# Optimization experiments

Hardware: AMD Instinct MI355X
Metric: run time of the kernel (lower is better)

The kernel has to match this reference:

```python
import jax, jax.numpy as jnp
import numpy as np

N, E = 20000, 320000
CS, CV = 64, 32            # 64x0e + 32x1o node irreps
CM = CS + CV               # mid scalar channels == mid vector channels == 96
WN = 2 * CS + 2 * CV       # tp weight numel per edge (4 uvu instructions) = 192
FCH = 64                   # fc hidden width
SQRT3 = 1.7320508075688772


def _fctp(s, v, attr, Ws, Wv):
    # FullyConnectedTensorProduct(x, attr='1x0e', out): per-l linear scaled by the scalar attr
    out_s = (s @ Ws) * attr / (s.shape[1] ** 0.5)
    out_v = jnp.einsum('nuc,uw->nwc', v, Wv) * attr[:, :, None] / (v.shape[1] ** 0.5)
    return out_s, out_v


def _fcnet(x, Wa, Wb):
    # FullyConnectedNet([64, 64, WN], silu)
    h = jax.nn.silu(x @ Wa / (x.shape[1] ** 0.5))
    return h @ Wb / (h.shape[1] ** 0.5)


def _conv(s, v, attr, edge_src, edge_dst, ea_s, ea_v, edge_scalars, inv_sqrt_deg, params):
    Wsc_s, Wsc_v, Wl1_s, Wl1_v, Wfa, Wfb, W2s, W2v, W3 = params
    n = s.shape[0]
    w = _fcnet(edge_scalars, Wfa, Wfb)                      # [E, 192] per-edge tp weights
    w00, w01, w10, w11 = w[:, :CS], w[:, CS:2 * CS], w[:, 2 * CS:2 * CS + CV], w[:, 2 * CS + CV:]
    sc_s, sc_v = _fctp(s, v, attr, Wsc_s, Wsc_v)            # self connection
    f_s, f_v = _fctp(s, v, attr, Wl1_s, Wl1_v)              # lin1
    gs, gv = f_s[edge_src], f_v[edge_src]                   # gather by edge source
    # weighted CG tensor product (uvu), sorted irreps_mid = 96x0e + 96x1o
    mid_s = jnp.concatenate([
        w00 * gs * ea_s,                                    # 0e x 0e -> 0e
        w11 * jnp.einsum('euc,ec->eu', gv, ea_v) / SQRT3,   # 1o x 1o -> 0e
    ], axis=-1)                                             # [E, 96]
    mid_v = jnp.concatenate([
        (w01 * gs)[:, :, None] * ea_v[:, None, :],          # 0e x 1o -> 1o
        w10[:, :, None] * gv * ea_s[:, :, None],            # 1o x 0e -> 1o
    ], axis=1)                                              # [E, 96, 3]
    agg_s = jax.ops.segment_sum(mid_s, edge_dst, num_segments=n) * inv_sqrt_deg
    agg_v = jax.ops.segment_sum(mid_v, edge_dst, num_segments=n) * inv_sqrt_deg[:, :, None]
    fan = CM ** 0.5
    out_s = (agg_s @ W2s) * attr / fan                      # lin2
    out_v = jnp.einsum('nuc,uw->nwc', agg_v, W2v) * attr[:, :, None] / fan
    angle = 0.1 * (agg_s @ W3) * attr / fan                 # lin3 -> '0e'
    c, si = jnp.cos(angle), jnp.sin(angle)                  # sc output_mask is all-ones here
    return c * sc_s + si * out_s, c[:, :, None] * sc_v + si[:, :, None] * out_v


def _forward(node_features, node_attr, edge_attr, edge_scalars, edge_src, edge_dst, params1, params2):
    n = node_features.shape[0]
    s = node_features[:, :CS]
    v = node_features[:, CS:].reshape(n, CV, 3)
    ea_s, ea_v = edge_attr[:, :1], edge_attr[:, 1:4]
    deg = jax.ops.segment_sum(jnp.ones((edge_dst.shape[0],), node_features.dtype), edge_dst, num_segments=n)
    inv_sqrt_deg = (1.0 / jnp.sqrt(deg))[:, None]           # every node has >= 1 in-edge by construction
    h_s, h_v = _conv(s, v, node_attr, edge_src, edge_dst, ea_s, ea_v, edge_scalars, inv_sqrt_deg, params1)
    # Gate: 64x0e scalars (silu) + 32x0e gates (sigmoid) gating 32x1o
    g_s = jax.nn.silu(h_s[:, :CS])
    g_v = jax.nn.sigmoid(h_s[:, CS:CS + CV])[:, :, None] * h_v
    o_s, o_v = _conv(g_s, g_v, node_attr, edge_src, edge_dst, ea_s, ea_v, edge_scalars, inv_sqrt_deg, params2)
    return jnp.concatenate([o_s, o_v.reshape(n, CV * 3)], axis=-1)


def setup_inputs():
    key = jax.random.key(0)
    ks = jax.random.split(key, 24)
    inp = {
        'node_features': jax.random.normal(ks[0], (N, CS + 3 * CV), jnp.float32),
        'node_attr': jnp.ones((N, 1), jnp.float32),
        'edge_src': jax.random.randint(ks[1], (E,), 0, N, dtype=jnp.int32),
        'edge_dst': jnp.concatenate([jnp.arange(N, dtype=jnp.int32),
                                     jax.random.randint(ks[2], (E - N,), 0, N, dtype=jnp.int32)]),
        'edge_attr': jax.random.normal(ks[3], (E, 4), jnp.float32),
        'edge_scalars': jax.random.normal(ks[4], (E, CS), jnp.float32),
    }
    shapes = {
        'p1_sc_s': (CS, CS + CV), 'p1_sc_v': (CV, CV),
        'p1_l1_s': (CS, CS), 'p1_l1_v': (CV, CV),
        'p1_fa': (CS, FCH), 'p1_fb': (FCH, WN),
        'p1_l2_s': (CM, CS + CV), 'p1_l2_v': (CM, CV), 'p1_l3': (CM, 1),
        'p2_sc_s': (CS, CS), 'p2_sc_v': (CV, CV),
        'p2_l1_s': (CS, CS), 'p2_l1_v': (CV, CV),
        'p2_fa': (CS, FCH), 'p2_fb': (FCH, WN),
        'p2_l2_s': (CM, CS), 'p2_l2_v': (CM, CV), 'p2_l3': (CM, 1),
    }
    for i, (name, shp) in enumerate(shapes.items()):
        inp[name] = jax.random.normal(ks[5 + i], shp, jnp.float32)
    return inp


def reference(node_features, node_attr, edge_attr, edge_scalars, edge_src, edge_dst,
              p1_sc_s, p1_sc_v, p1_l1_s, p1_l1_v, p1_fa, p1_fb, p1_l2_s, p1_l2_v, p1_l3,
              p2_sc_s, p2_sc_v, p2_l1_s, p2_l1_v, p2_fa, p2_fb, p2_l2_s, p2_l2_v, p2_l3):
    params1 = (p1_sc_s, p1_sc_v, p1_l1_s, p1_l1_v, p1_fa, p1_fb, p1_l2_s, p1_l2_v, p1_l3)
    params2 = (p2_sc_s, p2_sc_v, p2_l1_s, p2_l1_v, p2_fa, p2_fb, p2_l2_s, p2_l2_v, p2_l3)
    return _forward(node_features, node_attr, edge_attr, edge_scalars, edge_src, edge_dst, params1, params2)
```

## Files before the change

### kernel.cpp

```cpp
#include <hip/hip_runtime.h>
#include <hip/hip_fp16.h>
#include <cstdint>


#define CS 64
#define CV 32
#define CM 96
#define WN 192
#define FCH 64
#define WPAD 72
#define CHUNK 64
#define NSLABS 2

using f16x8 = __attribute__((ext_vector_type(8))) _Float16;
using f32x4 = __attribute__((ext_vector_type(4))) float;

__device__ __forceinline__ float siluf(float x){ return x / (1.f + __expf(-x)); }

constexpr float INV8       = 0.125f;
constexpr float INV_SQRT32 = 0.17677669529663687f;
constexpr float INV_SQRT96 = 0.10206207261596575f;
constexpr float INV_SQRT3  = 0.5773502691896258f;

__global__ void hist_kernel(const int* __restrict__ edst, int* __restrict__ cnt, int E){
    int e = blockIdx.x*blockDim.x + threadIdx.x;
    if (e < E) atomicAdd(&cnt[edst[e]], 1);
}

__global__ void scan_kernel(const int* __restrict__ cnt, int* __restrict__ row_start,
                            int* __restrict__ cursor, int n, int E){
    __shared__ int part[1024];
    const int t = threadIdx.x;
    const int C = (n + 1023) / 1024;
    int local[32];
    int base = t*C;
    int s = 0;
    for (int j = 0; j < C && j < 32; ++j){
        int idx = base + j;
        int v = (idx < n) ? cnt[idx] : 0;
        local[j] = s; s += v;
    }
    part[t] = s;
    __syncthreads();
    for (int off = 1; off < 1024; off <<= 1){
        int v = (t >= off) ? part[t-off] : 0;
        __syncthreads();
        part[t] += v;
        __syncthreads();
    }
    int pre = (t == 0) ? 0 : part[t-1];
    for (int j = 0; j < C && j < 32; ++j){
        int idx = base + j;
        if (idx < n){ int rs = pre + local[j]; row_start[idx] = rs; cursor[idx] = rs; }
    }
    if (t == 0) row_start[n] = E;
}

__global__ void scatter_kernel(const int* __restrict__ edst, const int* __restrict__ esrc,
                               const float4* __restrict__ eattr,
                               int* __restrict__ cursor, int* __restrict__ perm,
                               float4* __restrict__ eattr_s, int* __restrict__ esrc_s, int E){
    int e = blockIdx.x*blockDim.x + threadIdx.x;
    if (e < E){
        int p = atomicAdd(&cursor[edst[e]], 1);
        perm[p] = e; eattr_s[p] = eattr[e]; esrc_s[p] = esrc[e];
    }
}

__global__ void isd_kernel(const int* __restrict__ cnt, float* __restrict__ isd, int n){
    int i = blockIdx.x*blockDim.x + threadIdx.x;
    if (i < n) isd[i] = rsqrtf((float)cnt[i]);
}

__global__ void wprep(const float* __restrict__ Wfa1, const float* __restrict__ Wfb1,
                      const float* __restrict__ Wfa2, const float* __restrict__ Wfb2,
                      __half* __restrict__ Wc1, __half* __restrict__ Wc2){
    int t = blockIdx.x*blockDim.x + threadIdx.x;
    if (t < 64*WPAD){
        int c = t / WPAD, k = t - c*WPAD;
        float v1 = (k < 64) ? Wfa1[k*64 + c]*INV8 : 0.f;
        float v2 = (k < 64) ? Wfa2[k*64 + c]*INV8 : 0.f;
        Wc1[t] = __float2half(v1); Wc2[t] = __float2half(v2);
    } else if (t < 64*WPAD + 192*WPAD){
        int q = t - 64*WPAD; int o = q / WPAD, k = q - o*WPAD;
        float v1 = (k < 64) ? Wfb1[k*192 + o]*INV8 : 0.f;
        float v2 = (k < 64) ? Wfb2[k*192 + o]*INV8 : 0.f;
        Wc1[t] = __float2half(v1); Wc2[t] = __float2half(v2);
    }
}

__global__ void wprep_pre(
    const float* __restrict__ l1s1, const float* __restrict__ scs1,
    const float* __restrict__ l1v1, const float* __restrict__ scv1,
    const float* __restrict__ l1s2, const float* __restrict__ scs2,
    const float* __restrict__ l1v2, const float* __restrict__ scv2,
    __half* __restrict__ Bs1, __half* __restrict__ Bs2,
    __half* __restrict__ Bv1, __half* __restrict__ Bv2)
{
    int t = blockIdx.x*blockDim.x + threadIdx.x;
    if (t < 160*72){
        int col = t/72, k = t - col*72;
        float v = 0.f;
        if (k < 64) v = (col < 64 ? l1s1[k*64 + col] : scs1[k*96 + (col-64)]) * INV8;
        Bs1[t] = __float2half(v);
    } else if (t < 160*72 + 128*72){
        int q = t - 160*72; int col = q/72, k = q - col*72;
        float v = 0.f;
        if (k < 64) v = (col < 64 ? l1s2[k*64 + col] : scs2[k*64 + (col-64)]) * INV8;
        Bs2[q] = __float2half(v);
    } else if (t < 160*72 + 128*72 + 64*40){
        int q = t - (160*72 + 128*72); int col = q/40, k = q - col*40;
        float v = 0.f;
        if (k < 32) v = (col < 32 ? l1v1[k*32 + col] : scv1[k*32 + (col-32)]) * INV_SQRT32;
        Bv1[q] = __float2half(v);
    } else if (t < 160*72 + 128*72 + 2*64*40){
        int q = t - (160*72 + 128*72 + 64*40); int col = q/40, k = q - col*40;
        float v = 0.f;
        if (k < 32) v = (col < 32 ? l1v2[k*32 + col] : scv2[k*32 + (col-32)]) * INV_SQRT32;
        Bv2[q] = __float2half(v);
    }
}

template<int OS>
__global__ __launch_bounds__(256) void node_pre_mfma(
    const float* __restrict__ s, int ss,
    const float* __restrict__ v, int vs,
    const float* __restrict__ attr,
    const __half* __restrict__ Bs, const __half* __restrict__ Bv,
    __half* __restrict__ f_s, float* __restrict__ sc_s,
    __half* __restrict__ f_v, float* __restrict__ sc_v, int N)
{
    constexpr int SC = 64 + OS;
    __shared__ __align__(16) __half sAh[64*168];
    __shared__ __align__(16) __half lBs[SC*72];
    __shared__ __align__(16) __half lBv[64*40];
    __shared__ float s_at[64];

    const int tid = threadIdx.x;
    const int n0 = blockIdx.x*64;
    const int nmax = min(64, N - n0);

    for (int i = tid; i < (SC*72)/8; i += 256)
        reinterpret_cast<uint4*>(lBs)[i] = reinterpret_cast<const uint4*>(Bs)[i];
    for (int i = tid; i < (64*40)/8; i += 256)
        reinterpret_cast<uint4*>(lBv)[i] = reinterpret_cast<const uint4*>(Bv)[i];
    for (int i = tid; i < 64*64; i += 256){
        int n = i >> 6, k = i & 63;
        float x = (n < nmax) ? s[(size_t)(n0+n)*ss + k] : 0.f;
        sAh[n*168 + k] = __float2half(x);
    }
    for (int i = tid; i < 64*96; i += 256){
        int n = i/96, k = i - n*96;
        float x = (n < nmax) ? v[(size_t)(n0+n)*vs + k] : 0.f;
        sAh[n*168 + 64 + k] = __float2half(x);
    }
    if (tid < 64) s_at[tid] = (tid < nmax) ? attr[n0 + tid] : 0.f;
    __syncthreads();

    const int wv = tid >> 6, l = tid & 63;
    const int lm = l & 15, kg = l >> 4;
    const int rbase = wv*16;
    const int orow = rbase + kg*4;

    f16x8 xf0 = *reinterpret_cast<const f16x8*>(&sAh[(rbase+lm)*168 + kg*8]);
    f16x8 xf1 = *reinterpret_cast<const f16x8*>(&sAh[(rbase+lm)*168 + 32 + kg*8]);
    #pragma unroll
    for (int nt = 0; nt < SC/16; ++nt){
        f16x8 wb0 = *reinterpret_cast<const f16x8*>(&lBs[(nt*16+lm)*72 + kg*8]);
        f16x8 wb1 = *reinterpret_cast<const f16x8*>(&lBs[(nt*16+lm)*72 + 32 + kg*8]);
        f32x4 acc = {0.f,0.f,0.f,0.f};
        acc = __builtin_amdgcn_mfma_f32_16x16x32_f16(xf0, wb0, acc, 0, 0, 0);
        acc = __builtin_amdgcn_mfma_f32_16x16x32_f16(xf1, wb1, acc, 0, 0, 0);
        const int col = nt*16 + lm;
        #pragma unroll
        for (int r = 0; r < 4; ++r){
            int nl = orow + r;
            if (nl < nmax){
                float val = acc[r]*s_at[nl];
                if (col < 64) f_s[(size_t)(n0+nl)*64 + col] = __float2half(val);
                else          sc_s[(size_t)(n0+nl)*OS + (col-64)] = val;
            }
        }
    }

    #pragma unroll
    for (int c = 0; c < 3; ++c){
        f16x8 xa;
        #pragma unroll
        for (int j = 0; j < 8; ++j)
            xa[j] = (_Float16)sAh[(rbase+lm)*168 + 64 + (kg*8+j)*3 + c];
        #pragma unroll
        for (int nt = 0; nt < 4; ++nt){
            f16x8 wb = *reinterpret_cast<const f16x8*>(&lBv[(nt*16+lm)*40 + kg*8]);
            f32x4 acc = {0.f,0.f,0.f,0.f};
            acc = __builtin_amdgcn_mfma_f32_16x16x32_f16(xa, wb, acc, 0, 0, 0);
            const int col = nt*16 + lm;
            #pragma unroll
            for (int r = 0; r < 4; ++r){
                int nl = orow + r;
                if (nl < nmax){
                    float val = acc[r]*s_at[nl];
                    if (col < 32) f_v[(size_t)(n0+nl)*96 + col*3 + c] = __float2half(val);
                    else          sc_v[(size_t)(n0+nl)*96 + (col-32)*3 + c] = val;
                }
            }
        }
    }
}

__global__ __launch_bounds__(256) void mlp_gemm_slab(
    const int* __restrict__ row_start, int n0, int n1,
    const int* __restrict__ perm, const float* __restrict__ escal,
    const __half* __restrict__ Wc, __half* __restrict__ w_slab, int E)
{
    __shared__ __half lWa[64*WPAD];
    __shared__ __half lWb[192*WPAD];
    __shared__ __half hsm[4][16*WPAD];

    const int rs_slab = row_start[n0];
    const int re_slab = row_start[n1];
    if (rs_slab + (int)blockIdx.x*64 >= re_slab) return;

    const int tid = threadIdx.x;
    {
        const uint4* src4 = reinterpret_cast<const uint4*>(Wc);
        uint4* dA = reinterpret_cast<uint4*>(lWa);
        uint4* dB = reinterpret_cast<uint4*>(lWb);
        for (int i = tid; i < (64*WPAD)/8; i += 256) dA[i] = src4[i];
        for (int i = tid; i < (192*WPAD)/8; i += 256) dB[i] = src4[(64*WPAD)/8 + i];
    }
    __syncthreads();

    const int wv = tid >> 6, l = tid & 63;
    const int lm = l & 15, kg = l >> 4;

    for (int tile = rs_slab + blockIdx.x*64; tile < re_slab; tile += gridDim.x*64){
        const int base = tile + wv*16;
        int slot = base + lm; if (slot >= re_slab) slot = re_slab - 1;
        const int e = perm[slot];
        const float* xp = escal + (size_t)e*64 + kg*8;
        f16x8 xf0, xf1;
        {
            float4 a0 = *reinterpret_cast<const float4*>(xp);
            float4 a1 = *reinterpret_cast<const float4*>(xp + 4);
            float4 b0 = *reinterpret_cast<const float4*>(xp + 32);
            float4 b1 = *reinterpret_cast<const float4*>(xp + 36);
            xf0[0]=(_Float16)a0.x; xf0[1]=(_Float16)a0.y; xf0[2]=(_Float16)a0.z; xf0[3]=(_Float16)a0.w;
            xf0[4]=(_Float16)a1.x; xf0[5]=(_Float16)a1.y; xf0[6]=(_Float16)a1.z; xf0[7]=(_Float16)a1.w;
            xf1[0]=(_Float16)b0.x; xf1[1]=(_Float16)b0.y; xf1[2]=(_Float16)b0.z; xf1[3]=(_Float16)b0.w;
            xf1[4]=(_Float16)b1.x; xf1[5]=(_Float16)b1.y; xf1[6]=(_Float16)b1.z; xf1[7]=(_Float16)b1.w;
        }

        #pragma unroll
        for (int nt = 0; nt < 4; ++nt){
            f16x8 wa0 = *reinterpret_cast<const f16x8*>(&lWa[(nt*16 + lm)*WPAD + kg*8]);
            f16x8 wa1 = *reinterpret_cast<const f16x8*>(&lWa[(nt*16 + lm)*WPAD + 32 + kg*8]);
            f32x4 acc = {0.f,0.f,0.f,0.f};
            acc = __builtin_amdgcn_mfma_f32_16x16x32_f16(xf0, wa0, acc, 0, 0, 0);
            acc = __builtin_amdgcn_mfma_f32_16x16x32_f16(xf1, wa1, acc, 0, 0, 0);
            #pragma unroll
            for (int r = 0; r < 4; ++r)
                hsm[wv][(kg*4 + r)*WPAD + nt*16 + lm] = __float2half(siluf(acc[r]));
        }
        f16x8 ha0 = *reinterpret_cast<const f16x8*>(&hsm[wv][lm*WPAD + kg*8]);
        f16x8 ha1 = *reinterpret_cast<const f16x8*>(&hsm[wv][lm*WPAD + 32 + kg*8]);
        const int orow = base + kg*4;
        #pragma unroll 4
        for (int nt = 0; nt < 12; ++nt){
            f16x8 wb0 = *reinterpret_cast<const f16x8*>(&lWb[(nt*16 + lm)*WPAD + kg*8]);
            f16x8 wb1 = *reinterpret_cast<const f16x8*>(&lWb[(nt*16 + lm)*WPAD + 32 + kg*8]);
            f32x4 acc = {0.f,0.f,0.f,0.f};
            acc = __builtin_amdgcn_mfma_f32_16x16x32_f16(ha0, wb0, acc, 0, 0, 0);
            acc = __builtin_amdgcn_mfma_f32_16x16x32_f16(ha1, wb1, acc, 0, 0, 0);
            #pragma unroll
            for (int r = 0; r < 4; ++r){
                int row = orow + r;
                if (row < re_slab)
                    w_slab[(size_t)(row - rs_slab)*WN + nt*16 + lm] = __float2half(acc[r]);
            }
        }
    }
}

__global__ __launch_bounds__(384) void agg_slab(
    const int* __restrict__ row_start, int n0, const __half* __restrict__ w_slab,
    const int* __restrict__ esrc_s, const float4* __restrict__ eattr_s,
    const __half* __restrict__ f_s, const __half* __restrict__ f_v,
    float* __restrict__ aggs, float* __restrict__ aggv, int N)
{
    const int n = n0 + blockIdx.x;
    if (n >= N) return;
    const int t = threadIdx.x;
    const int rs_slab = row_start[n0];
    const int rs = row_start[n], re = row_start[n+1];
    const size_t N96 = (size_t)N*96;

    int widx, fidx, mode, eac = 0;
    float* outp;
    if (t < 64){ widx = t; fidx = t; mode = 0; eac = 0; outp = aggs + (size_t)n*96 + t; }
    else if (t < 256){ int j = t-64; int c = j>>6; int u = j&63;
        widx = 64+u; fidx = u; mode = 0; eac = 1+c; outp = aggv + (size_t)c*N96 + (size_t)n*96 + u; }
    else if (t < 352){ int j = t-256; int c = j>>5; int u = j&31;
        widx = 128+u; fidx = 3*u+c; mode = 2; outp = aggv + (size_t)c*N96 + (size_t)n*96 + 64+u; }
    else { int u = t-352; widx = 160+u; fidx = 3*u; mode = 1; outp = aggs + (size_t)n*96 + 64+u; }

    __shared__ int   s_src[CHUNK];
    __shared__ float s_ea[4][CHUNK];

    float acc = 0.f;
    for (int c0 = rs; c0 < re; c0 += CHUNK){
        const int m = min(CHUNK, re - c0);
        __syncthreads();
        if (t < m){
            s_src[t] = esrc_s[c0 + t];
            float4 ea = eattr_s[c0 + t];
            s_ea[0][t] = ea.x; s_ea[1][t] = ea.y;
            s_ea[2][t] = ea.z; s_ea[3][t] = ea.w;
        }
        __syncthreads();

        const __half* wp = w_slab + (size_t)(c0 - rs_slab)*WN + widx;
        if (mode == 0){
            int i = 0;
            for (; i + 8 <= m; i += 8){
                float w8[8], g8[8], e8[8];
                #pragma unroll
                for (int k = 0; k < 8; ++k) w8[k] = __half2float(wp[(i+k)*WN]);
                #pragma unroll
                for (int k = 0; k < 8; ++k) g8[k] = __half2float(f_s[(size_t)s_src[i+k]*64 + fidx]);
                #pragma unroll
                for (int k = 0; k < 8; ++k) e8[k] = s_ea[eac][i+k];
                #pragma unroll
                for (int k = 0; k < 8; ++k) acc += w8[k]*g8[k]*e8[k];
            }
            for (; i < m; ++i)
                acc += __half2float(wp[i*WN]) * __half2float(f_s[(size_t)s_src[i]*64 + fidx]) * s_ea[eac][i];
        } else if (mode == 2){
            int i = 0;
            for (; i + 8 <= m; i += 8){
                float w8[8], g8[8], e8[8];
                #pragma unroll
                for (int k = 0; k < 8; ++k) w8[k] = __half2float(wp[(i+k)*WN]);
                #pragma unroll
                for (int k = 0; k < 8; ++k) g8[k] = __half2float(f_v[(size_t)s_src[i+k]*96 + fidx]);
                #pragma unroll
                for (int k = 0; k < 8; ++k) e8[k] = s_ea[0][i+k];
                #pragma unroll
                for (int k = 0; k < 8; ++k) acc += w8[k]*g8[k]*e8[k];
            }
            for (; i < m; ++i)
                acc += __half2float(wp[i*WN]) * __half2float(f_v[(size_t)s_src[i]*96 + fidx]) * s_ea[0][i];
        } else {
            int i = 0;
            for (; i + 4 <= m; i += 4){
                float w4[4], d4[4];
                #pragma unroll
                for (int k = 0; k < 4; ++k) w4[k] = __half2float(wp[(i+k)*WN]);
                #pragma unroll
                for (int k = 0; k < 4; ++k){
                    const __half* p = f_v + (size_t)s_src[i+k]*96 + fidx;
                    d4[k] = __half2float(p[0])*s_ea[1][i+k] + __half2float(p[1])*s_ea[2][i+k]
                          + __half2float(p[2])*s_ea[3][i+k];
                }
                #pragma unroll
                for (int k = 0; k < 4; ++k) acc += w4[k]*d4[k];
            }
            for (; i < m; ++i){
                const __half* p = f_v + (size_t)s_src[i]*96 + fidx;
                float d = __half2float(p[0])*s_ea[1][i] + __half2float(p[1])*s_ea[2][i]
                        + __half2float(p[2])*s_ea[3][i];
                acc += __half2float(wp[i*WN]) * d;
            }
            acc *= INV_SQRT3;
        }
    }
    *outp = acc;
}

template<int OS, bool FINAL>
__global__ __launch_bounds__(256) void post_fused(
    const float* __restrict__ aggs, const float* __restrict__ aggv,
    const float* __restrict__ W2s, const float* __restrict__ W2v,
    const float* __restrict__ W3,
    const float* __restrict__ isd, const float* __restrict__ attr,
    const float* __restrict__ sc_s, const float* __restrict__ sc_v,
    float* __restrict__ out_s, float* __restrict__ out_v, int N)
{
    constexpr int TOTC = OS + 1 + 96;
    constexpr int PSTR = 96*8 + 8;
    __shared__ __align__(16) float s_a[4*PSTR];
    __shared__ float s_pre[8][TOTC];

    const int t = threadIdx.x;
    const int n0 = blockIdx.x*8;
    const int nmax = min(8, N - n0);
    const size_t N96 = (size_t)N*96;

    for (int idx = t; idx < 8*96; idx += 256){
        int n = idx/96, k = idx - n*96;
        if (n < nmax) s_a[k*8 + n] = aggs[(size_t)(n0+n)*96 + k];
    }
    for (int idx = t; idx < 3*8*96; idx += 256){
        int p = idx/768, rem = idx - p*768;
        int n = rem/96, k = rem - n*96;
        if (n < nmax) s_a[(1+p)*PSTR + k*8 + n] = aggv[(size_t)p*N96 + (size_t)(n0+n)*96 + k];
    }
    __syncthreads();

    if (t < TOTC){
        const float* bp; int bstr; int plane;
        if (t < OS){ bp = W2s + t; bstr = OS; plane = 0; }
        else if (t == OS){ bp = W3; bstr = 1; plane = 0; }
        else { int q = t - OS - 1; int cv = q>>5, ww = q&31; bp = W2v + ww; bstr = 32; plane = 1+cv; }
        const float* ap = &s_a[plane*PSTR];

        float acc0=0,acc1=0,acc2=0,acc3=0,acc4=0,acc5=0,acc6=0,acc7=0;
        #pragma unroll 4
        for (int k = 0; k < 96; ++k){
            float b = bp[(size_t)k*bstr];
            float4 q0 = *reinterpret_cast<const float4*>(ap + k*8);
            float4 q1 = *reinterpret_cast<const float4*>(ap + k*8 + 4);
            acc0 += q0.x*b; acc1 += q0.y*b; acc2 += q0.z*b; acc3 += q0.w*b;
            acc4 += q1.x*b; acc5 += q1.y*b; acc6 += q1.z*b; acc7 += q1.w*b;
        }
        s_pre[0][t]=acc0; s_pre[1][t]=acc1; s_pre[2][t]=acc2; s_pre[3][t]=acc3;
        s_pre[4][t]=acc4; s_pre[5][t]=acc5; s_pre[6][t]=acc6; s_pre[7][t]=acc7;
    }
    __syncthreads();

    for (int idx = t; idx < nmax*192; idx += 256){
        int n = idx/192, r = idx - n*192;
        int gn = n0 + n;
        float sca = isd[gn]*attr[gn]*INV_SQRT96;
        float ang = 0.1f * s_pre[n][OS] * sca;
        float c_ = cosf(ang), s_ = sinf(ang);
        if (r < OS){
            float hs = c_*sc_s[(size_t)gn*OS + r] + s_*s_pre[n][r]*sca;
            if (FINAL) out_s[(size_t)gn*160 + r] = hs;
            else if (r < 64) out_s[(size_t)gn*64 + r] = siluf(hs);
        } else if (r >= 96){
            int q2 = r - 96;
            int ww = q2/3, c2 = q2 - 3*ww;
            float hv = c_*sc_v[(size_t)gn*96 + q2] + s_*s_pre[n][OS+1 + c2*32 + ww]*sca;
            if (FINAL){
                out_s[(size_t)gn*160 + 64 + q2] = hv;
            } else {
                float hs64 = c_*sc_s[(size_t)gn*OS + 64 + ww] + s_*s_pre[n][64 + ww]*sca;
                float sg = 1.f/(1.f + __expf(-hs64));
                out_v[(size_t)gn*96 + q2] = sg*hv;
            }
        }
    }
}

extern "C" void kernel_launch(void* const* d_in, const int* in_sizes, int n_in,
                              void* d_out, int out_size, void* d_ws, size_t ws_size,
                              hipStream_t stream)
{
    const float* nf    = (const float*)d_in[0];
    const float* nattr = (const float*)d_in[1];
    const int*   esrc  = (const int*)  d_in[2];
    const int*   edst  = (const int*)  d_in[3];
    const float* eattr = (const float*)d_in[4];
    const float* escal = (const float*)d_in[5];
    const float* p1_sc_s = (const float*)d_in[6];
    const float* p1_sc_v = (const float*)d_in[7];
    const float* p1_l1_s = (const float*)d_in[8];
    const float* p1_l1_v = (const float*)d_in[9];
    const float* p1_fa   = (const float*)d_in[10];
    const float* p1_fb   = (const float*)d_in[11];
    const float* p1_l2_s = (const float*)d_in[12];
    const float* p1_l2_v = (const float*)d_in[13];
    const float* p1_l3   = (const float*)d_in[14];
    const float* p2_sc_s = (const float*)d_in[15];
    const float* p2_sc_v = (const float*)d_in[16];
    const float* p2_l1_s = (const float*)d_in[17];
    const float* p2_l1_v = (const float*)d_in[18];
    const float* p2_fa   = (const float*)d_in[19];
    const float* p2_fb   = (const float*)d_in[20];
    const float* p2_l2_s = (const float*)d_in[21];
    const float* p2_l2_v = (const float*)d_in[22];
    const float* p2_l3   = (const float*)d_in[23];

    const int N = in_sizes[1];
    const int E = in_sizes[2];

    char* wsb = (char*)d_ws;
    __half* w_s     = (__half*)wsb;   wsb += (size_t)E*WN*2;
    float4* eattr_s = (float4*)wsb;   wsb += (size_t)E*16;
    __half* Wc1 = (__half*)wsb;       wsb += (size_t)(256*WPAD)*2;
    __half* Wc2 = (__half*)wsb;       wsb += (size_t)(256*WPAD)*2;
    __half* Bs1 = (__half*)wsb;       wsb += (size_t)(160*72)*2;
    __half* Bs2 = (__half*)wsb;       wsb += (size_t)(128*72)*2;
    __half* Bv1 = (__half*)wsb;       wsb += (size_t)(64*40)*2;
    __half* Bv2 = (__half*)wsb;       wsb += (size_t)(64*40)*2;
    __half* fs  = (__half*)wsb;       wsb += (size_t)N*64*2;
    __half* fv  = (__half*)wsb;       wsb += (size_t)N*96*2;
    float* scs  = (float*)wsb;        wsb += (size_t)N*96*4;
    float* scv  = (float*)wsb;        wsb += (size_t)N*96*4;
    float* gs   = (float*)wsb;        wsb += (size_t)N*64*4;
    float* gv   = (float*)wsb;        wsb += (size_t)N*96*4;
    float* aggs = (float*)wsb;        wsb += (size_t)N*96*4;
    float* aggv = (float*)wsb;        wsb += (size_t)N*96*3*4;
    float* isd  = (float*)wsb;        wsb += (size_t)N*4;
    int* cnt       = (int*)wsb;       wsb += (size_t)N*4;
    int* row_start = (int*)wsb;       wsb += (size_t)(N+1)*4;
    int* cursor    = (int*)wsb;       wsb += (size_t)N*4;
    int* perm      = (int*)wsb;       wsb += (size_t)E*4;
    int* esrc_s    = (int*)wsb;       wsb += (size_t)E*4;

    hipMemsetAsync(cnt, 0, (size_t)N*4, stream);
    hist_kernel<<<(E+255)/256, 256, 0, stream>>>(edst, cnt, E);
    scan_kernel<<<1, 1024, 0, stream>>>(cnt, row_start, cursor, N, E);
    scatter_kernel<<<(E+255)/256, 256, 0, stream>>>(edst, esrc, (const float4*)eattr,
                                                    cursor, perm, eattr_s, esrc_s, E);
    isd_kernel<<<(N+255)/256, 256, 0, stream>>>(cnt, isd, N);
    wprep<<<(256*WPAD+255)/256, 256, 0, stream>>>(p1_fa, p1_fb, p2_fa, p2_fb, Wc1, Wc2);
    wprep_pre<<<(160*72+128*72+2*64*40+255)/256, 256, 0, stream>>>(
        p1_l1_s, p1_sc_s, p1_l1_v, p1_sc_v,
        p2_l1_s, p2_sc_s, p2_l1_v, p2_sc_v, Bs1, Bs2, Bv1, Bv2);

    const int pre_grid  = (N + 63)/64;
    const int post_grid = (N + 7)/8;
    const int slabN = (N + NSLABS - 1)/NSLABS;
    const int mlp_grid = 768;

    node_pre_mfma<96><<<pre_grid, 256, 0, stream>>>(nf, 160, nf+64, 160, nattr,
        Bs1, Bv1, fs, scs, fv, scv, N);
    for (int s = 0; s < NSLABS; ++s){
        int n0 = s*slabN; if (n0 >= N) break;
        int n1 = (n0 + slabN < N) ? n0 + slabN : N;
        mlp_gemm_slab<<<mlp_grid, 256, 0, stream>>>(row_start, n0, n1, perm, escal,
                                                    Wc1, w_s, E);
        agg_slab<<<n1 - n0, 384, 0, stream>>>(row_start, n0, w_s,
                                              esrc_s, eattr_s, fs, fv, aggs, aggv, N);
    }
    post_fused<96, false><<<post_grid, 256, 0, stream>>>(aggs, aggv,
        p1_l2_s, p1_l2_v, p1_l3, isd, nattr, scs, scv, gs, gv, N);

    node_pre_mfma<64><<<pre_grid, 256, 0, stream>>>(gs, 64, gv, 96, nattr,
        Bs2, Bv2, fs, scs, fv, scv, N);
    for (int s = 0; s < NSLABS; ++s){
        int n0 = s*slabN; if (n0 >= N) break;
        int n1 = (n0 + slabN < N) ? n0 + slabN : N;
        mlp_gemm_slab<<<mlp_grid, 256, 0, stream>>>(row_start, n0, n1, perm, escal,
                                                    Wc2, w_s, E);
        agg_slab<<<n1 - n0, 384, 0, stream>>>(row_start, n0, w_s,
                                              esrc_s, eattr_s, fs, fv, aggs, aggv, N);
    }
    post_fused<64, true><<<post_grid, 256, 0, stream>>>(aggs, aggv,
        p2_l2_s, p2_l2_v, p2_l3, isd, nattr, scs, scv, (float*)d_out, nullptr, N);
}
```

Baseline: 475.9 us.

## Compute four outputs per thread in agg_slab to reuse gathered features

The aggregation kernel now runs 128 threads per node instead of 384. Each thread keeps four accumulators: scalar threads handle one channel for the 0e×0e output and all three 1o components from the same gathered f_s value, and vector threads handle the three 0e×1o components plus the dot-product scalar from one gathered 3-vector. This removes repeated gathers of the same source features and repeated shared-memory reads across threads. In exchange there are fewer threads per block, a third of them sit idle (threads 96–127), and each thread has more serial work, so latency hiding may drop.

New measurement: 385.8 us (median of 2 runs). -18.9%, faster.

```diff
diff --git a/kernel.cpp b/kernel.cpp
--- a/kernel.cpp
+++ b/kernel.cpp
@@ -282,7 +282,7 @@
     }
 }
 
-__global__ __launch_bounds__(384) void agg_slab(
+__global__ __launch_bounds__(128) void agg_slab(
     const int* __restrict__ row_start, int n0, const __half* __restrict__ w_slab,
     const int* __restrict__ esrc_s, const float4* __restrict__ eattr_s,
     const __half* __restrict__ f_s, const __half* __restrict__ f_v,
@@ -295,19 +295,14 @@
     const int rs = row_start[n], re = row_start[n+1];
     const size_t N96 = (size_t)N*96;
 
-    int widx, fidx, mode, eac = 0;
-    float* outp;
-    if (t < 64){ widx = t; fidx = t; mode = 0; eac = 0; outp = aggs + (size_t)n*96 + t; }
-    else if (t < 256){ int j = t-64; int c = j>>6; int u = j&63;
-        widx = 64+u; fidx = u; mode = 0; eac = 1+c; outp = aggv + (size_t)c*N96 + (size_t)n*96 + u; }
-    else if (t < 352){ int j = t-256; int c = j>>5; int u = j&31;
-        widx = 128+u; fidx = 3*u+c; mode = 2; outp = aggv + (size_t)c*N96 + (size_t)n*96 + 64+u; }
-    else { int u = t-352; widx = 160+u; fidx = 3*u; mode = 1; outp = aggs + (size_t)n*96 + 64+u; }
-
     __shared__ int   s_src[CHUNK];
     __shared__ float s_ea[4][CHUNK];
 
-    float acc = 0.f;
+    const bool isScalar = (t < 64);
+    const int u = t - 64;
+
+    float a0 = 0.f, a1 = 0.f, a2 = 0.f, a3 = 0.f;
+
     for (int c0 = rs; c0 < re; c0 += CHUNK){
         const int m = min(CHUNK, re - c0);
         __syncthreads();
@@ -319,62 +314,91 @@
         }
         __syncthreads();
 
-        const __half* wp = w_slab + (size_t)(c0 - rs_slab)*WN + widx;
-        if (mode == 0){
-            int i = 0;
-            for (; i + 8 <= m; i += 8){
-                float w8[8], g8[8], e8[8];
-                #pragma unroll
-                for (int k = 0; k < 8; ++k) w8[k] = __half2float(wp[(i+k)*WN]);
-                #pragma unroll
-                for (int k = 0; k < 8; ++k) g8[k] = __half2float(f_s[(size_t)s_src[i+k]*64 + fidx]);
-                #pragma unroll
-                for (int k = 0; k < 8; ++k) e8[k] = s_ea[eac][i+k];
-                #pragma unroll
-                for (int k = 0; k < 8; ++k) acc += w8[k]*g8[k]*e8[k];
-            }
-            for (; i < m; ++i)
-                acc += __half2float(wp[i*WN]) * __half2float(f_s[(size_t)s_src[i]*64 + fidx]) * s_ea[eac][i];
-        } else if (mode == 2){
-            int i = 0;
-            for (; i + 8 <= m; i += 8){
-                float w8[8], g8[8], e8[8];
-                #pragma unroll
-                for (int k = 0; k < 8; ++k) w8[k] = __half2float(wp[(i+k)*WN]);
-                #pragma unroll
-                for (int k = 0; k < 8; ++k) g8[k] = __half2float(f_v[(size_t)s_src[i+k]*96 + fidx]);
-                #pragma unroll
-                for (int k = 0; k < 8; ++k) e8[k] = s_ea[0][i+k];
-                #pragma unroll
-                for (int k = 0; k < 8; ++k) acc += w8[k]*g8[k]*e8[k];
-            }
-            for (; i < m; ++i)
-                acc += __half2float(wp[i*WN]) * __half2float(f_v[(size_t)s_src[i]*96 + fidx]) * s_ea[0][i];
-        } else {
+        const __half* wp = w_slab + (size_t)(c0 - rs_slab)*WN;
+
+        if (isScalar){
             int i = 0;
             for (; i + 4 <= m; i += 4){
-                float w4[4], d4[4];
-                #pragma unroll
-                for (int k = 0; k < 4; ++k) w4[k] = __half2float(wp[(i+k)*WN]);
+                float w0[4], w1[4], g[4];
+                int   s4[4];
+                #pragma unroll
+                for (int k = 0; k < 4; ++k) s4[k] = s_src[i+k];
+                #pragma unroll
+                for (int k = 0; k < 4; ++k) w0[k] = __half2float(wp[(size_t)(i+k)*WN + t]);
+                #pragma unroll
+                for (int k = 0; k < 4; ++k) w1[k] = __half2float(wp[(size_t)(i+k)*WN + 64 + t]);
+                #pragma unroll
+                for (int k = 0; k < 4; ++k) g[k]  = __half2float(f_s[(size_t)s4[k]*64 + t]);
                 #pragma unroll
                 for (int k = 0; k < 4; ++k){
-                    const __half* p = f_v + (size_t)s_src[i+k]*96 + fidx;
-                    d4[k] = __half2float(p[0])*s_ea[1][i+k] + __half2float(p[1])*s_ea[2][i+k]
-                          + __half2float(p[2])*s_ea[3][i+k];
+                    float wg = w1[k]*g[k];
+                    a0 += w0[k]*g[k]*s_ea[0][i+k];
+                    a1 += wg*s_ea[1][i+k];
+                    a2 += wg*s_ea[2][i+k];
+                    a3 += wg*s_ea[3][i+k];
                 }
-                #pragma unroll
-                for (int k = 0; k < 4; ++k) acc += w4[k]*d4[k];
             }
             for (; i < m; ++i){
-                const __half* p = f_v + (size_t)s_src[i]*96 + fidx;
-                float d = __half2float(p[0])*s_ea[1][i] + __half2float(p[1])*s_ea[2][i]
-                        + __half2float(p[2])*s_ea[3][i];
-                acc += __half2float(wp[i*WN]) * d;
-            }
-            acc *= INV_SQRT3;
-        }
-    }
-    *outp = acc;
+                int src = s_src[i];
+                float w0 = __half2float(wp[(size_t)i*WN + t]);
+                float w1 = __half2float(wp[(size_t)i*WN + 64 + t]);
+                float g  = __half2float(f_s[(size_t)src*64 + t]);
+                float wg = w1*g;
+                a0 += w0*g*s_ea[0][i];
+                a1 += wg*s_ea[1][i];
+                a2 += wg*s_ea[2][i];
+                a3 += wg*s_ea[3][i];
+            }
+        } else if (u < 32){
+            int i = 0;
+            for (; i + 4 <= m; i += 4){
+                float w2[4], w3[4], f0[4], f1[4], f2[4];
+                int s4[4];
+                #pragma unroll
+                for (int k = 0; k < 4; ++k) s4[k] = s_src[i+k];
+                #pragma unroll
+                for (int k = 0; k < 4; ++k) w2[k] = __half2float(wp[(size_t)(i+k)*WN + 128 + u]);
+                #pragma unroll
+                for (int k = 0; k < 4; ++k) w3[k] = __half2float(wp[(size_t)(i+k)*WN + 160 + u]);
+                #pragma unroll
+                for (int k = 0; k < 4; ++k){
+                    const __half* p = f_v + (size_t)s4[k]*96 + 3*u;
+                    f0[k] = __half2float(p[0]); f1[k] = __half2float(p[1]); f2[k] = __half2float(p[2]);
+                }
+                #pragma unroll
+                for (int k = 0; k < 4; ++k){
+                    float eax = s_ea[0][i+k];
+                    float w2e = w2[k]*eax;
+                    a0 += w2e*f0[k];
+                    a1 += w2e*f1[k];
+                    a2 += w2e*f2[k];
+                    a3 += w3[k]*(f0[k]*s_ea[1][i+k] + f1[k]*s_ea[2][i+k] + f2[k]*s_ea[3][i+k]);
+                }
+            }
+            for (; i < m; ++i){
+                int src = s_src[i];
+                float w2 = __half2float(wp[(size_t)i*WN + 128 + u]);
+                float w3 = __half2float(wp[(size_t)i*WN + 160 + u]);
+                const __half* p = f_v + (size_t)src*96 + 3*u;
+                float f0 = __half2float(p[0]), f1 = __half2float(p[1]), f2 = __half2float(p[2]);
+                float w2e = w2*s_ea[0][i];
+                a0 += w2e*f0; a1 += w2e*f1; a2 += w2e*f2;
+                a3 += w3*(f0*s_ea[1][i] + f1*s_ea[2][i] + f2*s_ea[3][i]);
+            }
+        }
+    }
+
+    if (isScalar){
+        aggs[(size_t)n*96 + t] = a0;
+        aggv[(size_t)0*N96 + (size_t)n*96 + t] = a1;
+        aggv[(size_t)1*N96 + (size_t)n*96 + t] = a2;
+        aggv[(size_t)2*N96 + (size_t)n*96 + t] = a3;
+    } else if (u < 32){
+        aggv[(size_t)0*N96 + (size_t)n*96 + 64 + u] = a0;
+        aggv[(size_t)1*N96 + (size_t)n*96 + 64 + u] = a1;
+        aggv[(size_t)2*N96 + (size_t)n*96 + 64 + u] = a2;
+        aggs[(size_t)n*96 + 64 + u] = a3*INV_SQRT3;
+    }
 }
 
 template<int OS, bool FINAL>
@@ -532,7 +556,7 @@
         int n1 = (n0 + slabN < N) ? n0 + slabN : N;
         mlp_gemm_slab<<<mlp_grid, 256, 0, stream>>>(row_start, n0, n1, perm, escal,
                                                     Wc1, w_s, E);
-        agg_slab<<<n1 - n0, 384, 0, stream>>>(row_start, n0, w_s,
+        agg_slab<<<n1 - n0, 128, 0, stream>>>(row_start, n0, w_s,
                                               esrc_s, eattr_s, fs, fv, aggs, aggv, N);
     }
     post_fused<96, false><<<post_grid, 256, 0, stream>>>(aggs, aggv,
@@ -545,7 +569,7 @@
         int n1 = (n0 + slabN < N) ? n0 + slabN : N;
         mlp_gemm_slab<<<mlp_grid, 256, 0, stream>>>(row_start, n0, n1, perm, escal,
                                                     Wc2, w_s, E);
-        agg_slab<<<n1 - n0, 384, 0, stream>>>(row_start, n0, w_s,
+        agg_slab<<<n1 - n0, 128, 0, stream>>>(row_start, n0, w_s,
                                               esrc_s, eattr_s, fs, fv, aggs, aggv, N);
     }
     post_fused<64, true><<<post_grid, 256, 0, stream>>>(aggs, aggv,
```
